# Optimization experiments

Hardware: AMD Instinct MI355X
Metric: run time of the kernel (lower is better)

The kernel has to match this reference:

```python
import jax, jax.numpy as jnp
import numpy as np

EMB_DIM = 256
NUM_HEADS = 4
HEAD_DIM = EMB_DIM // NUM_HEADS
N_EDGES = 320000
N_NODES = 10000
EPS = 1e-16  # torch_geometric softmax epsilon


def setup_inputs() -> dict:
    key = jax.random.key(0)
    kq, kk, ki, kw1, kb1, kw2 = jax.random.split(key, 6)
    q = jax.random.normal(kq, (N_EDGES, EMB_DIM), dtype=jnp.float32)
    k = jax.random.normal(kk, (N_EDGES, EMB_DIM), dtype=jnp.float32)
    index = jnp.sort(jax.random.randint(ki, (N_EDGES,), 0, N_NODES, dtype=jnp.int32))
    # xavier_uniform with gain 1/sqrt(2)
    lim1 = (1.0 / np.sqrt(2.0)) * np.sqrt(6.0 / (2 * EMB_DIM + EMB_DIM))
    w1_w = jax.random.uniform(kw1, (EMB_DIM, 2 * EMB_DIM), dtype=jnp.float32, minval=-lim1, maxval=lim1)
    w1_b = jnp.zeros((EMB_DIM,), dtype=jnp.float32)
    lim2 = (1.0 / np.sqrt(2.0)) * np.sqrt(6.0 / (NUM_HEADS + HEAD_DIM))
    w2 = jax.random.uniform(kw2, (NUM_HEADS, HEAD_DIM), dtype=jnp.float32, minval=-lim2, maxval=lim2)
    return {"q": q, "k": k, "w1_w": w1_w, "w1_b": w1_b, "w2": w2,
            "index": index, "dim_size": N_NODES}


def _segment_softmax(src, index, num_segments):
    # src: [E, H, 1]; index: [E] segment ids; stable softmax per segment per head
    seg_max = jax.ops.segment_max(src, index, num_segments=num_segments)  # [N, H, 1]
    out = jnp.exp(src - seg_max[index])
    seg_sum = jax.ops.segment_sum(out, index, num_segments=num_segments)  # [N, H, 1]
    return out / (seg_sum[index] + EPS)


def reference(q, k, w1_w, w1_b, w2, index, dim_size):
    x = jnp.concatenate([q, k], axis=1)                      # [E, 2D]
    x = x @ w1_w.T + w1_b                                    # [E, D]
    x = jax.nn.leaky_relu(x, negative_slope=0.01)
    x = x.reshape(-1, NUM_HEADS, HEAD_DIM)                   # [E, H, C]
    attn = jnp.einsum('nhc,hc->nh', x, w2)[..., None]        # [E, H, 1]
    return _segment_softmax(attn, index, dim_size)
```

## Files before the change

### kernel.cpp

```cpp
#include <hip/hip_runtime.h>
#include <hip/hip_bf16.h>


typedef __attribute__((ext_vector_type(8))) short bf16x8;
typedef __attribute__((ext_vector_type(4))) float f32x4;
typedef __attribute__((ext_vector_type(4))) short s16x4;

#define NNODES 10000

__device__ __forceinline__ short f2bf(float f) {
    __hip_bfloat16 h = __float2bfloat16(f);
    return *reinterpret_cast<short*>(&h);
}

__device__ __forceinline__ void gload_lds16(const void* g, void* l) {
    __builtin_amdgcn_global_load_lds(
        (const __attribute__((address_space(1))) unsigned int*)g,
        (__attribute__((address_space(3))) unsigned int*)l, 16, 0, 0);
}

__global__ void w1_cvt(const float* __restrict__ w1, short* __restrict__ w1b) {
    int i = (blockIdx.x * 256 + threadIdx.x) * 4;
    float4 v = *(const float4*)(w1 + i);
    s16x4 o; o[0] = f2bf(v.x); o[1] = f2bf(v.y); o[2] = f2bf(v.z); o[3] = f2bf(v.w);
    *(s16x4*)(w1b + i) = o;
}

__global__ void seg_init(float* __restrict__ segsum, int n) {
    int i = blockIdx.x * blockDim.x + threadIdx.x;
    if (i < n) segsum[i] = 0.f;
}

__global__ __launch_bounds__(512, 4) void attn_gemm(
    const float* __restrict__ q, const float* __restrict__ kk_,
    const short* __restrict__ w1b, const float* __restrict__ b1,
    const float* __restrict__ w2, const int* __restrict__ index,
    float* __restrict__ attn, float* __restrict__ segsum)
{
    __shared__ short lds_a[2][128 * 32];
    __shared__ short lds_b[2][256 * 32];

    const int tid  = threadIdx.x;
    const int lane = tid & 63;
    const int w    = tid >> 6;
    const int wm   = w >> 2;
    const int wn   = w & 3;
    const int l15  = lane & 15;
    const int lhi  = lane >> 4;
    const int row0 = blockIdx.x * 128;

    const int b_d    = w * 16 + (lane >> 2);
    const int b_csrc = (lane & 3) ^ ((lane >> 3) & 3);
    const size_t b_off0 = (size_t)b_d * 512 + b_csrc * 8;
    const size_t b_off1 = (size_t)(128 + b_d) * 512 + b_csrc * 8;
    const int b_dst0 = w * 1024 + lane * 16;
    const int b_dst1 = (8 + w) * 1024 + lane * 16;

    const int a_r = tid >> 2;
    const int a_c = tid & 3;
    const size_t a_goff = (size_t)(row0 + a_r) * 256 + a_c * 8;
    const int a_ldst = a_r * 32 + ((a_c ^ ((a_r >> 1) & 3)) * 8);

    f32x4 acc[4][4];
#pragma unroll
    for (int i = 0; i < 4; ++i)
#pragma unroll
        for (int j = 0; j < 4; ++j) acc[i][j] = (f32x4){0.f, 0.f, 0.f, 0.f};

    {
        gload_lds16(w1b + b_off0, (char*)&lds_b[0][0] + b_dst0);
        gload_lds16(w1b + b_off1, (char*)&lds_b[0][0] + b_dst1);
        float4 f0 = *(const float4*)(q + a_goff);
        float4 f1 = *(const float4*)(q + a_goff + 4);
        bf16x8 pk;
        pk[0] = f2bf(f0.x); pk[1] = f2bf(f0.y); pk[2] = f2bf(f0.z); pk[3] = f2bf(f0.w);
        pk[4] = f2bf(f1.x); pk[5] = f2bf(f1.y); pk[6] = f2bf(f1.z); pk[7] = f2bf(f1.w);
        *(bf16x8*)&lds_a[0][a_ldst] = pk;
    }
    __syncthreads();

#pragma unroll
    for (int kt = 0; kt < 16; ++kt) {
        const int cur = kt & 1, nxt = cur ^ 1;

        float4 f0, f1;
        if (kt < 15) {
            const float* abase = (kt + 1 < 8) ? q : kk_;
            const int koff = ((kt + 1) & 7) * 32;
            f0 = *(const float4*)(abase + a_goff + koff);
            f1 = *(const float4*)(abase + a_goff + koff + 4);
            gload_lds16(w1b + b_off0 + (size_t)(kt + 1) * 32, (char*)&lds_b[nxt][0] + b_dst0);
            gload_lds16(w1b + b_off1 + (size_t)(kt + 1) * 32, (char*)&lds_b[nxt][0] + b_dst1);
        }

        bf16x8 af[4], bfv[4];
#pragma unroll
        for (int fm = 0; fm < 4; ++fm) {
            const int r = wm * 64 + fm * 16 + l15;
            af[fm] = *(const bf16x8*)&lds_a[cur][r * 32 + ((lhi ^ ((r >> 1) & 3)) * 8)];
        }
#pragma unroll
        for (int fn = 0; fn < 4; ++fn) {
            const int d = wn * 64 + fn * 16 + l15;
            bfv[fn] = *(const bf16x8*)&lds_b[cur][d * 32 + ((lhi ^ ((d >> 1) & 3)) * 8)];
        }
#pragma unroll
        for (int fm = 0; fm < 4; ++fm)
#pragma unroll
            for (int fn = 0; fn < 4; ++fn)
                acc[fm][fn] = __builtin_amdgcn_mfma_f32_16x16x32_bf16(
                    af[fm], bfv[fn], acc[fm][fn], 0, 0, 0);

        if (kt < 15) {
            bf16x8 pk;
            pk[0] = f2bf(f0.x); pk[1] = f2bf(f0.y); pk[2] = f2bf(f0.z); pk[3] = f2bf(f0.w);
            pk[4] = f2bf(f1.x); pk[5] = f2bf(f1.y); pk[6] = f2bf(f1.z); pk[7] = f2bf(f1.w);
            *(bf16x8*)&lds_a[nxt][a_ldst] = pk;
        }
        __syncthreads();
    }

    float bias[4], w2v[4];
#pragma unroll
    for (int fn = 0; fn < 4; ++fn) {
        int col = wn * 64 + fn * 16 + l15;
        bias[fn] = b1[col];
        w2v[fn]  = w2[col];
    }
#pragma unroll
    for (int fm = 0; fm < 4; ++fm) {
#pragma unroll
        for (int r = 0; r < 4; ++r) {
            int row = row0 + wm * 64 + fm * 16 + lhi * 4 + r;
            float p = 0.f;
#pragma unroll
            for (int fn = 0; fn < 4; ++fn) {
                float y = acc[fm][fn][r] + bias[fn];
                y = (y > 0.f) ? y : 0.01f * y;
                p += y * w2v[fn];
            }
#pragma unroll
            for (int m = 1; m < 16; m <<= 1) p += __shfl_xor(p, m);
            if (l15 == 0) {
                float e = __expf(p);
                attn[(size_t)row * 4 + wn] = e;
                atomicAdd(&segsum[index[row] * 4 + wn], e);
            }
        }
    }
}

__global__ void seg_norm(const float* __restrict__ attn, const int* __restrict__ index,
                         const float* __restrict__ segsum, float* __restrict__ out, int total) {
    int i = blockIdx.x * blockDim.x + threadIdx.x;
    if (i >= total) return;
    int e = i >> 2, h = i & 3;
    out[i] = attn[i] / (segsum[index[e] * 4 + h] + 1e-16f);
}

extern "C" void kernel_launch(void* const* d_in, const int* in_sizes, int n_in,
                              void* d_out, int out_size, void* d_ws, size_t ws_size,
                              hipStream_t stream) {
    const float* q   = (const float*)d_in[0];
    const float* k   = (const float*)d_in[1];
    const float* w1  = (const float*)d_in[2];
    const float* b1  = (const float*)d_in[3];
    const float* w2  = (const float*)d_in[4];
    const int* index = (const int*)d_in[5];

    const int nE = in_sizes[0] / 256;
    char* ws = (char*)d_ws;
    float* attn   = (float*)ws;            ws += (size_t)nE * 4 * 4;
    float* segsum = (float*)ws;            ws += (size_t)NNODES * 4 * 4;
    short* w1bf   = (short*)ws;
    float* out    = (float*)d_out;

    w1_cvt<<<128, 256, 0, stream>>>(w1, w1bf);
    seg_init<<<(NNODES * 4 + 255) / 256, 256, 0, stream>>>(segsum, NNODES * 4);

    attn_gemm<<<nE / 128, 512, 0, stream>>>(q, k, w1bf, b1, w2, index, attn, segsum);

    int total = nE * 4;
    seg_norm<<<(total + 255) / 256, 256, 0, stream>>>(attn, index, segsum, out, total);
}
```

Measured before the change: 230.0 us.

## Retile GEMM to 64-row blocks with K=64 stages and dynamic LDS

The fused GEMM kernel now uses 256-thread blocks of four waves, each computing a 64x64 output slice over 64 rows, instead of 512 threads over 128 rows. Each K stage covers 64 columns, so there are 8 iterations and half as many barriers. A is prefetched two stages ahead in registers, B is staged into 80KB of dynamic LDS with an 8-way XOR swizzle, and the kernel launches twice as many blocks. This trades W1 reuse per block and occupancy (larger LDS footprint) for fewer synchronisations and deeper prefetching of the memory-bound fp32 activation stream.

```diff
diff --git a/kernel.cpp b/kernel.cpp
--- a/kernel.cpp
+++ b/kernel.cpp
@@ -31,35 +31,31 @@
     if (i < n) segsum[i] = 0.f;
 }
 
-__global__ __launch_bounds__(512, 4) void attn_gemm(
+__global__ __launch_bounds__(256, 2) void attn_gemm(
     const float* __restrict__ q, const float* __restrict__ kk_,
     const short* __restrict__ w1b, const float* __restrict__ b1,
     const float* __restrict__ w2, const int* __restrict__ index,
     float* __restrict__ attn, float* __restrict__ segsum)
 {
-    __shared__ short lds_a[2][128 * 32];
-    __shared__ short lds_b[2][256 * 32];
+    extern __shared__ __align__(16) short smem[];
+    short* const ldsA[2] = { smem, smem + 4096 };
+    short* const ldsB[2] = { smem + 8192, smem + 24576 };
 
     const int tid  = threadIdx.x;
     const int lane = tid & 63;
-    const int w    = tid >> 6;
-    const int wm   = w >> 2;
-    const int wn   = w & 3;
+    const int wn   = tid >> 6;
     const int l15  = lane & 15;
     const int lhi  = lane >> 4;
-    const int row0 = blockIdx.x * 128;
-
-    const int b_d    = w * 16 + (lane >> 2);
-    const int b_csrc = (lane & 3) ^ ((lane >> 3) & 3);
-    const size_t b_off0 = (size_t)b_d * 512 + b_csrc * 8;
-    const size_t b_off1 = (size_t)(128 + b_d) * 512 + b_csrc * 8;
-    const int b_dst0 = w * 1024 + lane * 16;
-    const int b_dst1 = (8 + w) * 1024 + lane * 16;
-
-    const int a_r = tid >> 2;
-    const int a_c = tid & 3;
-    const size_t a_goff = (size_t)(row0 + a_r) * 256 + a_c * 8;
-    const int a_ldst = a_r * 32 + ((a_c ^ ((a_r >> 1) & 3)) * 8);
+    const int row0 = blockIdx.x * 64;
+
+    const int rt = tid >> 2, ct = tid & 3;
+    const size_t a_goff = (size_t)(row0 + rt) * 256 + ct * 16;
+    const int a_wb0 = rt * 128 + (((ct * 2 + 0) ^ (rt & 7)) << 4);
+    const int a_wb1 = rt * 128 + (((ct * 2 + 1) ^ (rt & 7)) << 4);
+
+    const int b_d    = tid >> 3;
+    const int b_csrc = (tid & 7) ^ ((tid >> 3) & 7);
+    const size_t b_goff = (size_t)b_d * 512 + b_csrc * 8;
 
     f32x4 acc[4][4];
 #pragma unroll
@@ -67,58 +63,78 @@
 #pragma unroll
         for (int j = 0; j < 4; ++j) acc[i][j] = (f32x4){0.f, 0.f, 0.f, 0.f};
 
-    {
-        gload_lds16(w1b + b_off0, (char*)&lds_b[0][0] + b_dst0);
-        gload_lds16(w1b + b_off1, (char*)&lds_b[0][0] + b_dst1);
-        float4 f0 = *(const float4*)(q + a_goff);
-        float4 f1 = *(const float4*)(q + a_goff + 4);
-        bf16x8 pk;
-        pk[0] = f2bf(f0.x); pk[1] = f2bf(f0.y); pk[2] = f2bf(f0.z); pk[3] = f2bf(f0.w);
-        pk[4] = f2bf(f1.x); pk[5] = f2bf(f1.y); pk[6] = f2bf(f1.z); pk[7] = f2bf(f1.w);
-        *(bf16x8*)&lds_a[0][a_ldst] = pk;
-    }
+    float4 ar[2][4];
+
+#define STAGE_B(kt, buf) {                                                      \
+        char* bB = (char*)ldsB[buf];                                            \
+        _Pragma("unroll")                                                       \
+        for (int i2 = 0; i2 < 8; ++i2)                                          \
+            gload_lds16(w1b + (size_t)i2 * 32 * 512 + b_goff + (kt) * 64,       \
+                        bB + (i2 * 256 + tid) * 16);                            \
+    }
+#define LOADA(j) {                                                              \
+        const float* bp = ((j) < 4) ? q : kk_;                                  \
+        const float* p  = bp + a_goff + ((j) & 3) * 64;                         \
+        ar[(j) & 1][0] = *(const float4*)p;                                     \
+        ar[(j) & 1][1] = *(const float4*)(p + 4);                               \
+        ar[(j) & 1][2] = *(const float4*)(p + 8);                               \
+        ar[(j) & 1][3] = *(const float4*)(p + 12);                              \
+    }
+#define WRITE_A(j, buf) {                                                       \
+        bf16x8 p0, p1;                                                          \
+        float4 v0 = ar[(j) & 1][0], v1 = ar[(j) & 1][1];                        \
+        float4 v2 = ar[(j) & 1][2], v3 = ar[(j) & 1][3];                        \
+        p0[0]=f2bf(v0.x); p0[1]=f2bf(v0.y); p0[2]=f2bf(v0.z); p0[3]=f2bf(v0.w); \
+        p0[4]=f2bf(v1.x); p0[5]=f2bf(v1.y); p0[6]=f2bf(v1.z); p0[7]=f2bf(v1.w); \
+        p1[0]=f2bf(v2.x); p1[1]=f2bf(v2.y); p1[2]=f2bf(v2.z); p1[3]=f2bf(v2.w); \
+        p1[4]=f2bf(v3.x); p1[5]=f2bf(v3.y); p1[6]=f2bf(v3.z); p1[7]=f2bf(v3.w); \
+        *(bf16x8*)((char*)ldsA[buf] + a_wb0) = p0;                              \
+        *(bf16x8*)((char*)ldsA[buf] + a_wb1) = p1;                              \
+    }
+
+    STAGE_B(0, 0);
+    LOADA(0);
+    WRITE_A(0, 0);
+    LOADA(1);
     __syncthreads();
 
 #pragma unroll
-    for (int kt = 0; kt < 16; ++kt) {
+    for (int kt = 0; kt < 8; ++kt) {
         const int cur = kt & 1, nxt = cur ^ 1;
-
-        float4 f0, f1;
-        if (kt < 15) {
-            const float* abase = (kt + 1 < 8) ? q : kk_;
-            const int koff = ((kt + 1) & 7) * 32;
-            f0 = *(const float4*)(abase + a_goff + koff);
-            f1 = *(const float4*)(abase + a_goff + koff + 4);
-            gload_lds16(w1b + b_off0 + (size_t)(kt + 1) * 32, (char*)&lds_b[nxt][0] + b_dst0);
-            gload_lds16(w1b + b_off1 + (size_t)(kt + 1) * 32, (char*)&lds_b[nxt][0] + b_dst1);
+        if (kt < 7) STAGE_B(kt + 1, nxt);
+        if (kt < 6) LOADA(kt + 2);
+
+#pragma unroll
+        for (int ks = 0; ks < 2; ++ks) {
+            bf16x8 bfr[4], afr[4];
+#pragma unroll
+            for (int fn = 0; fn < 4; ++fn) {
+                const int d = wn * 64 + fn * 16 + l15;
+                bfr[fn] = *(const bf16x8*)((const char*)ldsB[cur] + d * 128 +
+                           (((ks * 4 + lhi) ^ (d & 7)) << 4));
+            }
+#pragma unroll
+            for (int fm = 0; fm < 4; ++fm) {
+                const int r = fm * 16 + l15;
+                afr[fm] = *(const bf16x8*)((const char*)ldsA[cur] + r * 128 +
+                           (((ks * 4 + lhi) ^ (r & 7)) << 4));
+            }
+#pragma unroll
+            for (int fm = 0; fm < 4; ++fm)
+#pragma unroll
+                for (int fn = 0; fn < 4; ++fn)
+                    acc[fm][fn] = __builtin_amdgcn_mfma_f32_16x16x32_bf16(
+                        afr[fm], bfr[fn], acc[fm][fn], 0, 0, 0);
         }
 
-        bf16x8 af[4], bfv[4];
-#pragma unroll
-        for (int fm = 0; fm < 4; ++fm) {
-            const int r = wm * 64 + fm * 16 + l15;
-            af[fm] = *(const bf16x8*)&lds_a[cur][r * 32 + ((lhi ^ ((r >> 1) & 3)) * 8)];
+        if (kt < 7) {
+            WRITE_A(kt + 1, nxt);
+            __syncthreads();
         }
-#pragma unroll
-        for (int fn = 0; fn < 4; ++fn) {
-            const int d = wn * 64 + fn * 16 + l15;
-            bfv[fn] = *(const bf16x8*)&lds_b[cur][d * 32 + ((lhi ^ ((d >> 1) & 3)) * 8)];
-        }
-#pragma unroll
-        for (int fm = 0; fm < 4; ++fm)
-#pragma unroll
-            for (int fn = 0; fn < 4; ++fn)
-                acc[fm][fn] = __builtin_amdgcn_mfma_f32_16x16x32_bf16(
-                    af[fm], bfv[fn], acc[fm][fn], 0, 0, 0);
-
-        if (kt < 15) {
-            bf16x8 pk;
-            pk[0] = f2bf(f0.x); pk[1] = f2bf(f0.y); pk[2] = f2bf(f0.z); pk[3] = f2bf(f0.w);
-            pk[4] = f2bf(f1.x); pk[5] = f2bf(f1.y); pk[6] = f2bf(f1.z); pk[7] = f2bf(f1.w);
-            *(bf16x8*)&lds_a[nxt][a_ldst] = pk;
-        }
-        __syncthreads();
-    }
+    }
+#undef STAGE_B
+#undef LOADA
+#undef WRITE_A
 
     float bias[4], w2v[4];
 #pragma unroll
@@ -131,7 +147,7 @@
     for (int fm = 0; fm < 4; ++fm) {
 #pragma unroll
         for (int r = 0; r < 4; ++r) {
-            int row = row0 + wm * 64 + fm * 16 + lhi * 4 + r;
+            int row = row0 + fm * 16 + lhi * 4 + r;
             float p = 0.f;
 #pragma unroll
             for (int fn = 0; fn < 4; ++fn) {
@@ -175,10 +191,13 @@
     short* w1bf   = (short*)ws;
     float* out    = (float*)d_out;
 
+    hipFuncSetAttribute((const void*)attn_gemm,
+                        hipFuncAttributeMaxDynamicSharedMemorySize, 81920);
+
     w1_cvt<<<128, 256, 0, stream>>>(w1, w1bf);
     seg_init<<<(NNODES * 4 + 255) / 256, 256, 0, stream>>>(segsum, NNODES * 4);
 
-    attn_gemm<<<nE / 128, 512, 0, stream>>>(q, k, w1bf, b1, w2, index, attn, segsum);
+    attn_gemm<<<nE / 64, 256, 81920, stream>>>(q, k, w1bf, b1, w2, index, attn, segsum);
 
     int total = nE * 4;
     seg_norm<<<(total + 255) / 256, 256, 0, stream>>>(attn, index, segsum, out, total);
```

Result: slower. 283.2 us (+23.1%).
